# Kernel tuning notes

Hardware: AMD Instinct MI355X
Metric: run time of the kernel (lower is better)

## Reference

```python
import jax, jax.numpy as jnp
import numpy as np

N = 10000   # nodes
E = 40000   # edges
B = 250     # graphs (40 nodes each)
NODE_IN = 74
EDGE_IN = 12
H = 64      # hidden_feats
RD = 1024   # readout_feats


def setup_inputs() -> dict:
    key = jax.random.key(0)
    ks = jax.random.split(key, 32)
    w = lambda i, shape: jax.random.normal(ks[i], shape, jnp.float32) * 0.05
    inp = {
        'node_attr': jax.random.normal(ks[0], (N, NODE_IN), jnp.float32),
        'edge_attr': jax.random.normal(ks[1], (E, EDGE_IN), jnp.float32),
        'src': jax.random.randint(ks[2], (E,), 0, N, jnp.int32),
        'dst': jax.random.randint(ks[3], (E,), 0, N, jnp.int32),
        'graph_ids': (jnp.arange(N, dtype=jnp.int32) // (N // B)),
        'num_graphs': B,
        # project_node_feats: Linear(NODE_IN, H)
        'Wp': w(4, (H, NODE_IN)), 'bp': w(5, (H,)),
        # FALayer gate: Linear(2H, 1)
        'Wg': w(6, (1, 2 * H)), 'bg': w(7, (1,)),
        # edge_network: Linear(EDGE_IN + 1, H*H)
        'We': w(8, (H * H, EDGE_IN + 1)), 'be': w(9, (H * H,)),
        'nnconv_bias': w(10, (H,)),
        # GRU(H, H), single layer
        'gru_wih': w(11, (3 * H, H)), 'gru_whh': w(12, (3 * H, H)),
        'gru_bih': w(13, (3 * H,)), 'gru_bhh': w(14, (3 * H,)),
        # Set2Set LSTM: input 4H -> hidden 2H
        'lstm_wih': w(15, (8 * H, 4 * H)), 'lstm_whh': w(16, (8 * H, 2 * H)),
        'lstm_bih': w(17, (8 * H,)), 'lstm_bhh': w(18, (8 * H,)),
        # sparsify: Linear(4H, RD) + PReLU
        'Ws': w(19, (RD, 4 * H)), 'bs': w(20, (RD,)),
        'prelu_a': jnp.asarray(0.25, jnp.float32),
    }
    return inp


def _seg_softmax(e, ids, num):
    m = jax.ops.segment_max(e, ids, num_segments=num)
    ex = jnp.exp(e - m[ids])
    den = jax.ops.segment_sum(ex, ids, num_segments=num)
    return ex / den[ids]


def _forward(node_attr, edge_attr, src, dst, graph_ids, num_graphs,
             Wp, bp, Wg, bg, We, be, nnconv_bias,
             gru_wih, gru_whh, gru_bih, gru_bhh,
             lstm_wih, lstm_whh, lstm_bih, lstm_bhh,
             Ws, bs, prelu_a):
    n = node_attr.shape[0]
    h0 = jax.nn.relu(node_attr @ Wp.T + bp)            # (N, H)

    # FALayer (eval mode: dropout is identity)
    deg = jax.ops.segment_sum(jnp.ones(src.shape[0], node_attr.dtype), dst,
                              num_segments=n)           # in-degrees (N,)
    h2 = jnp.concatenate([h0[dst], h0[src]], axis=1)    # (E, 2H)
    t = jnp.tanh(h2 @ Wg.T + bg)[:, 0]                  # (E,)
    e_gate = 0.3 + t * deg[dst] * deg[src]              # (E,)
    efeat = jnp.concatenate([edge_attr, e_gate[:, None]], axis=-1)  # (E, EDGE_IN+1)

    # NNConv per-edge dynamic weights (edge_feats fixed across steps)
    W_edge = (efeat @ We.T + be).reshape(-1, H, H)      # (E, H, H)

    h = h0
    hid = h0  # GRU hidden state
    for _ in range(3):  # num_step_message_passing
        m = jnp.einsum('ei,eio->eo', h[src], W_edge)    # per-edge matvec
        agg = jax.ops.segment_sum(m, dst, num_segments=n) + nnconv_bias
        x = jax.nn.relu(agg)
        # torch GRU (gate order r, z, n)
        gi = x @ gru_wih.T + gru_bih
        gh = hid @ gru_whh.T + gru_bhh
        r = jax.nn.sigmoid(gi[:, :H] + gh[:, :H])
        z = jax.nn.sigmoid(gi[:, H:2 * H] + gh[:, H:2 * H])
        ng = jnp.tanh(gi[:, 2 * H:] + r * gh[:, 2 * H:])
        hid = (1.0 - z) * ng + z * hid
        h = hid

    feat = jnp.concatenate([h0, h], axis=1)             # (N, 2H)
    D = 2 * H

    # Set2Set readout (LSTM gate order i, f, g, o)
    q_star = jnp.zeros((num_graphs, 2 * D), feat.dtype)
    hl = jnp.zeros((num_graphs, D), feat.dtype)
    cl = jnp.zeros((num_graphs, D), feat.dtype)
    for _ in range(3):  # num_step_set2set
        g4 = q_star @ lstm_wih.T + lstm_bih + hl @ lstm_whh.T + lstm_bhh
        i = jax.nn.sigmoid(g4[:, :D])
        f = jax.nn.sigmoid(g4[:, D:2 * D])
        gg = jnp.tanh(g4[:, 2 * D:3 * D])
        o = jax.nn.sigmoid(g4[:, 3 * D:])
        cl = f * cl + i * gg
        hl = o * jnp.tanh(cl)
        q = hl                                           # (B, D)
        sc = jnp.sum(feat * q[graph_ids], axis=-1)       # (N,)
        alpha = _seg_softmax(sc, graph_ids, num_graphs)
        readout = jax.ops.segment_sum(feat * alpha[:, None], graph_ids,
                                      num_segments=num_graphs)  # (B, D)
        q_star = jnp.concatenate([q, readout], axis=-1)  # (B, 2D)

    out = q_star @ Ws.T + bs
    return jnp.where(out >= 0, out, prelu_a * out)       # PReLU


def reference(node_attr, edge_attr, src, dst, graph_ids, num_graphs,
              Wp, bp, Wg, bg, We, be, nnconv_bias,
              gru_wih, gru_whh, gru_bih, gru_bhh,
              lstm_wih, lstm_whh, lstm_bih, lstm_bhh,
              Ws, bs, prelu_a):
    return _forward(node_attr, edge_attr, src, dst, graph_ids, num_graphs,
                    Wp, bp, Wg, bg, We, be, nnconv_bias,
                    gru_wih, gru_whh, gru_bih, gru_bhh,
                    lstm_wih, lstm_whh, lstm_bih, lstm_bhh,
                    Ws, bs, prelu_a)
```

## Files before the change

kernel.cpp:

```cpp
#include <hip/hip_runtime.h>
#include <math.h>


#define H 64
#define NODE_IN 74
#define EDGE_IN 12
#define EF 14
#define GCAP 256
#define MGH 1088

__device__ __forceinline__ float sigmoidf(float x) {
    return 1.0f / (1.0f + expf(-x));
}

template<int AOP>
__global__ __launch_bounds__(256)
void gemm128_k(const float* __restrict__ A, int lda,
               const float* __restrict__ B, int ldb,
               float* __restrict__ C, int ldc,
               int M, int N, int K,
               const float* __restrict__ abias)
{
    __shared__ float sA[64][132];
    __shared__ float sB[64][68];

    const int tid = threadIdx.x;
    const int bm  = blockIdx.x * 128;
    const int bn  = blockIdx.y * 64;
    const int tx  = tid & 15;
    const int ty  = tid >> 4;

    float acc[8][4] = {{0.f}};

    for (int k0 = 0; k0 < K; k0 += 64) {
        #pragma unroll
        for (int t = 0; t < 8; ++t) {
            int idx = tid + t * 256;
            int r   = idx >> 4;
            int c   = (idx & 15) << 2;
            float4 v = {0.f, 0.f, 0.f, 0.f};
            int gm = bm + r;
            if (gm < M) {
                v = *reinterpret_cast<const float4*>(A + (size_t)gm * lda + (k0 + c));
                if (AOP == 1) {
                    v.x = fmaxf(v.x + abias[k0 + c + 0], 0.f);
                    v.y = fmaxf(v.y + abias[k0 + c + 1], 0.f);
                    v.z = fmaxf(v.z + abias[k0 + c + 2], 0.f);
                    v.w = fmaxf(v.w + abias[k0 + c + 3], 0.f);
                }
            }
            sA[c + 0][r] = v.x;
            sA[c + 1][r] = v.y;
            sA[c + 2][r] = v.z;
            sA[c + 3][r] = v.w;
        }
        #pragma unroll
        for (int t = 0; t < 4; ++t) {
            int idx = tid + t * 256;
            int r   = idx >> 4;
            int c   = (idx & 15) << 2;
            *reinterpret_cast<float4*>(&sB[r][c]) =
                *reinterpret_cast<const float4*>(B + (size_t)(k0 + r) * ldb + (bn + c));
        }
        __syncthreads();

        #pragma unroll
        for (int kk = 0; kk < 64; ++kk) {
            float4 a0 = *reinterpret_cast<const float4*>(&sA[kk][ty * 8]);
            float4 a1 = *reinterpret_cast<const float4*>(&sA[kk][ty * 8 + 4]);
            float4 bv = *reinterpret_cast<const float4*>(&sB[kk][tx * 4]);
            float ar[8] = {a0.x, a0.y, a0.z, a0.w, a1.x, a1.y, a1.z, a1.w};
            float br[4] = {bv.x, bv.y, bv.z, bv.w};
            #pragma unroll
            for (int i = 0; i < 8; ++i)
                #pragma unroll
                for (int j = 0; j < 4; ++j)
                    acc[i][j] = fmaf(ar[i], br[j], acc[i][j]);
        }
        __syncthreads();
    }

    #pragma unroll
    for (int i = 0; i < 8; ++i) {
        int gm = bm + ty * 8 + i;
        if (gm < M) {
            float4 v = {acc[i][0], acc[i][1], acc[i][2], acc[i][3]};
            *reinterpret_cast<float4*>(C + (size_t)gm * ldc + bn + tx * 4) = v;
        }
    }
}

template<int EOP>
__global__ __launch_bounds__(256)
void gemm_k(const float* __restrict__ A, int lda,
            const float* __restrict__ B, int ldb,
            float* __restrict__ C, int ldc,
            int M, int N, int K,
            const float* __restrict__ cbias,
            const float* __restrict__ prelu_a)
{
    __shared__ float sA[64][68];
    __shared__ float sB[64][68];

    const int tid = threadIdx.x;
    const int bm  = blockIdx.x * 64;
    const int bn  = blockIdx.y * 64;
    const int tx  = tid & 15;
    const int ty  = tid >> 4;

    float acc[4][4] = {{0.f}};

    for (int k0 = 0; k0 < K; k0 += 64) {
        #pragma unroll
        for (int t = 0; t < 4; ++t) {
            int idx = tid + t * 256;
            int r   = idx >> 4;
            int c   = (idx & 15) << 2;
            float4 v = {0.f, 0.f, 0.f, 0.f};
            int gm = bm + r;
            if (gm < M)
                v = *reinterpret_cast<const float4*>(A + (size_t)gm * lda + (k0 + c));
            sA[c + 0][r] = v.x;
            sA[c + 1][r] = v.y;
            sA[c + 2][r] = v.z;
            sA[c + 3][r] = v.w;
        }
        #pragma unroll
        for (int t = 0; t < 4; ++t) {
            int idx = tid + t * 256;
            int r   = idx >> 4;
            int c   = (idx & 15) << 2;
            *reinterpret_cast<float4*>(&sB[r][c]) =
                *reinterpret_cast<const float4*>(B + (size_t)(k0 + r) * ldb + (bn + c));
        }
        __syncthreads();

        #pragma unroll
        for (int kk = 0; kk < 64; ++kk) {
            float4 av = *reinterpret_cast<const float4*>(&sA[kk][ty * 4]);
            float4 bv = *reinterpret_cast<const float4*>(&sB[kk][tx * 4]);
            float ar[4] = {av.x, av.y, av.z, av.w};
            float br[4] = {bv.x, bv.y, bv.z, bv.w};
            #pragma unroll
            for (int i = 0; i < 4; ++i)
                #pragma unroll
                for (int j = 0; j < 4; ++j)
                    acc[i][j] = fmaf(ar[i], br[j], acc[i][j]);
        }
        __syncthreads();
    }

    float pa = (EOP == 1) ? prelu_a[0] : 0.f;
    #pragma unroll
    for (int i = 0; i < 4; ++i) {
        int gm = bm + ty * 4 + i;
        if (gm < M) {
            float4 v;
            float* vv = reinterpret_cast<float*>(&v);
            #pragma unroll
            for (int j = 0; j < 4; ++j) {
                float c = acc[i][j];
                if (EOP == 1) {
                    c += cbias[bn + tx * 4 + j];
                    c = (c >= 0.f) ? c : pa * c;
                }
                vv[j] = c;
            }
            *reinterpret_cast<float4*>(C + (size_t)gm * ldc + bn + tx * 4) = v;
        }
    }
}

__global__ __launch_bounds__(256)
void prep_all_k(const float* __restrict__ na, const float* __restrict__ Wp,
                const float* __restrict__ bp, float* __restrict__ h0,
                const float* __restrict__ We, const float* __restrict__ be,
                const float* __restrict__ wih, const float* __restrict__ whh,
                const float* __restrict__ lwih, const float* __restrict__ lwhh,
                const float* __restrict__ Ws,
                float* __restrict__ We2b, float* __restrict__ wihT,
                float* __restrict__ WlT, float* __restrict__ WsT,
                const int* __restrict__ dst, float* __restrict__ deg,
                int* __restrict__ icnt,
                const int* __restrict__ gid, int* __restrict__ gcnt,
                int* __restrict__ glist,
                int N, int E,
                int nb_h0, int nb_prep, int nb_deg)
{
    int b   = blockIdx.x;
    int tid = threadIdx.x;
    if (b < nb_h0) {
        int idx = b * 256 + tid;
        if (idx >= N * H) return;
        int n = idx >> 6, o = idx & 63;
        const float* x = na + (size_t)n * NODE_IN;
        const float* w = Wp + (size_t)o * NODE_IN;
        float acc = bp[o];
        #pragma unroll
        for (int k = 0; k < NODE_IN; ++k) acc = fmaf(x[k], w[k], acc);
        h0[idx] = fmaxf(acc, 0.f);
    } else if (b < nb_h0 + nb_prep) {
        int t = (b - nb_h0) * 256 + tid;
        if (t < 69632) {
            int i = t / MGH, j = t % MGH;
            float v;
            if (j < 896) {
                int k = j >> 6, o = j & 63;
                v = (k < 13) ? We[(size_t)(i * 64 + o) * 13 + k] : be[i * 64 + o];
            } else {
                int jj = j - 896;
                v = whh[(size_t)jj * 64 + i];
            }
            We2b[t] = v;
        } else if (t < 81920) {
            int u = t - 69632;
            int i = u / 192, j = u % 192;
            wihT[u] = wih[(size_t)j * 64 + i];
        } else if (t < 278528) {
            int u = t - 81920;
            int k = u >> 9, j = u & 511;
            WlT[u] = (k < 256) ? lwih[(size_t)j * 256 + k]
                               : lwhh[(size_t)j * 128 + (k - 256)];
        } else if (t < 540672) {
            int u = t - 278528;
            int k = u >> 10, j = u & 1023;
            WsT[u] = Ws[(size_t)j * 256 + k];
        }
    } else if (b < nb_h0 + nb_prep + nb_deg) {
        int e = (b - nb_h0 - nb_prep) * 256 + tid;
        if (e < E) {
            int d = dst[e];
            atomicAdd(&deg[d], 1.0f);
            atomicAdd(&icnt[d], 1);
        }
    } else {
        int n = (b - nb_h0 - nb_prep - nb_deg) * 256 + tid;
        if (n < N) {
            int g = gid[n];
            int p = atomicAdd(&gcnt[g], 1);
            if (p < GCAP) glist[(size_t)g * GCAP + p] = n;
        }
    }
}

__global__ __launch_bounds__(1024)
void scan_k(const int* __restrict__ icnt, int* __restrict__ row_ptr,
            int* __restrict__ cursor, int N)
{
    __shared__ int s[1024];
    __shared__ int carry;
    int tid = threadIdx.x;
    if (tid == 0) { carry = 0; row_ptr[0] = 0; }
    __syncthreads();
    for (int base = 0; base < N; base += 1024) {
        int i = base + tid;
        int v = (i < N) ? icnt[i] : 0;
        s[tid] = v;
        __syncthreads();
        for (int off = 1; off < 1024; off <<= 1) {
            int t = (tid >= off) ? s[tid - off] : 0;
            __syncthreads();
            s[tid] += t;
            __syncthreads();
        }
        int incl = s[tid] + carry;
        if (i < N) { row_ptr[i + 1] = incl; cursor[i] = incl - v; }
        __syncthreads();
        if (tid == 1023) carry = incl;
        __syncthreads();
    }
}

__global__ __launch_bounds__(256)
void gate_k(const float* __restrict__ h0, const float* __restrict__ ea,
            const int* __restrict__ src, const int* __restrict__ dst,
            const float* __restrict__ Wg, const float* __restrict__ bg,
            const float* __restrict__ deg, float* __restrict__ ef,
            int* __restrict__ cursor, int* __restrict__ csr_eid, int E)
{
    int e    = blockIdx.x * 4 + (threadIdx.x >> 6);
    int lane = threadIdx.x & 63;
    if (e >= E) return;
    int s = src[e], d = dst[e];
    float v = Wg[lane]      * h0[(size_t)d * H + lane]
            + Wg[H + lane]  * h0[(size_t)s * H + lane];
    #pragma unroll
    for (int off = 32; off; off >>= 1) v += __shfl_xor(v, off);
    if (lane < EF) {
        float out;
        if (lane < EDGE_IN) out = ea[(size_t)e * EDGE_IN + lane];
        else if (lane == EDGE_IN) {
            float t = tanhf(v + bg[0]);
            out = 0.3f + t * deg[d] * deg[s];
        } else out = 1.0f;
        ef[(size_t)e * EF + lane] = out;
    } else if (lane == EF) {
        int pos = atomicAdd(&cursor[d], 1);
        csr_eid[pos] = e;
    }
}

__global__ __launch_bounds__(256)
void agg_csr_k(const float* __restrict__ M, const float* __restrict__ ef,
               const int* __restrict__ src, const int* __restrict__ csr_eid,
               const int* __restrict__ row_ptr, float* __restrict__ agg, int N)
{
    int n    = blockIdx.x * 4 + (threadIdx.x >> 6);
    int lane = threadIdx.x & 63;
    if (n >= N) return;
    int p0 = row_ptr[n], p1 = row_ptr[n + 1];
    float a = 0.f;
    for (int p = p0; p < p1; ++p) {
        int e = csr_eid[p];
        int s = src[e];
        const float* Ms = M + (size_t)s * MGH + lane;
        const float* f  = ef + (size_t)e * EF;
        #pragma unroll
        for (int k = 0; k < EF; ++k) a = fmaf(f[k], Ms[k * H], a);
    }
    agg[(size_t)n * H + lane] = a;
}

__global__ __launch_bounds__(256)
void gru_k(const float* __restrict__ gi, const float* __restrict__ gh, int ghld,
           const float* __restrict__ bih, const float* __restrict__ bhh,
           const float* __restrict__ hin, float* __restrict__ hout, int N)
{
    int idx = blockIdx.x * 256 + threadIdx.x;
    if (idx >= N * H) return;
    int n = idx >> 6, o = idx & 63;
    const float* gin = gi + (size_t)n * 192;
    const float* ghn = gh + (size_t)n * ghld;
    float r  = sigmoidf(gin[o]       + bih[o]       + ghn[o]       + bhh[o]);
    float z  = sigmoidf(gin[64 + o]  + bih[64 + o]  + ghn[64 + o]  + bhh[64 + o]);
    float gn = ghn[128 + o] + bhh[128 + o];
    float ng = tanhf(gin[128 + o] + bih[128 + o] + r * gn);
    float hv = hin[idx];
    hout[idx] = (1.f - z) * ng + z * hv;
}

__global__ __launch_bounds__(64)
void att_k(const float* __restrict__ h0, const float* __restrict__ h,
           const float* __restrict__ g4,
           const float* __restrict__ lbih, const float* __restrict__ lbhh,
           float* __restrict__ cl,
           const int* __restrict__ glist, const int* __restrict__ gcnt,
           float* __restrict__ Acat)
{
    int b    = blockIdx.x;
    int lane = threadIdx.x;
    __shared__ float q[128];
    __shared__ float sc[GCAP];

    const float* g = g4 + (size_t)b * 512;
    #pragma unroll
    for (int t = 0; t < 2; ++t) {
        int d = lane + t * 64;
        float ii = sigmoidf(g[d]       + lbih[d]       + lbhh[d]);
        float ff = sigmoidf(g[128 + d] + lbih[128 + d] + lbhh[128 + d]);
        float gg = tanhf  (g[256 + d] + lbih[256 + d] + lbhh[256 + d]);
        float oo = sigmoidf(g[384 + d] + lbih[384 + d] + lbhh[384 + d]);
        float c  = ff * cl[(size_t)b * 128 + d] + ii * gg;
        cl[(size_t)b * 128 + d] = c;
        q[d] = oo * tanhf(c);
    }
    __syncthreads();

    int c = gcnt[b]; if (c > GCAP) c = GCAP;

    float lmax = -INFINITY;
    for (int i = lane; i < c; i += 64) {
        int n = glist[(size_t)b * GCAP + i];
        const float* f0 = h0 + (size_t)n * H;
        const float* f1 = h  + (size_t)n * H;
        float s = 0.f;
        #pragma unroll
        for (int j = 0; j < H; ++j) s = fmaf(f0[j], q[j], s);
        #pragma unroll
        for (int j = 0; j < H; ++j) s = fmaf(f1[j], q[H + j], s);
        sc[i] = s;
        lmax = fmaxf(lmax, s);
    }
    #pragma unroll
    for (int off = 32; off; off >>= 1) lmax = fmaxf(lmax, __shfl_xor(lmax, off));

    float lsum = 0.f;
    for (int i = lane; i < c; i += 64) {
        float e = expf(sc[i] - lmax);
        sc[i] = e;
        lsum += e;
    }
    #pragma unroll
    for (int off = 32; off; off >>= 1) lsum += __shfl_xor(lsum, off);
    __syncthreads();

    float inv = 1.f / lsum;
    float r0 = 0.f, r1 = 0.f;
    for (int i = 0; i < c; ++i) {
        int n = glist[(size_t)b * GCAP + i];
        float w = sc[i];
        r0 = fmaf(w, h0[(size_t)n * H + lane], r0);
        r1 = fmaf(w, h [(size_t)n * H + lane], r1);
    }
    float* A = Acat + (size_t)b * 384;
    A[lane]       = q[lane];
    A[64 + lane]  = q[64 + lane];
    A[128 + lane] = r0 * inv;
    A[192 + lane] = r1 * inv;
    A[256 + lane] = q[lane];
    A[320 + lane] = q[64 + lane];
}

extern "C" void kernel_launch(void* const* d_in, const int* in_sizes, int n_in,
                              void* d_out, int out_size, void* d_ws, size_t ws_size,
                              hipStream_t stream)
{
    (void)n_in; (void)ws_size;
    const float* node_attr = (const float*)d_in[0];
    const float* edge_attr = (const float*)d_in[1];
    const int*   src       = (const int*)d_in[2];
    const int*   dst       = (const int*)d_in[3];
    const int*   gid       = (const int*)d_in[4];
    const float* Wp        = (const float*)d_in[6];
    const float* bp        = (const float*)d_in[7];
    const float* Wg        = (const float*)d_in[8];
    const float* bg        = (const float*)d_in[9];
    const float* We        = (const float*)d_in[10];
    const float* be        = (const float*)d_in[11];
    const float* nb        = (const float*)d_in[12];
    const float* gwih      = (const float*)d_in[13];
    const float* gwhh      = (const float*)d_in[14];
    const float* gbih      = (const float*)d_in[15];
    const float* gbhh      = (const float*)d_in[16];
    const float* lwih      = (const float*)d_in[17];
    const float* lwhh      = (const float*)d_in[18];
    const float* lbih      = (const float*)d_in[19];
    const float* lbhh      = (const float*)d_in[20];
    const float* Ws        = (const float*)d_in[21];
    const float* bs        = (const float*)d_in[22];
    const float* pa        = (const float*)d_in[23];

    const int N = in_sizes[0] / NODE_IN;
    const int E = in_sizes[2];
    const int B = out_size / 1024;

    float* ws = (float*)d_ws;
    size_t off = 0;
    auto alloc = [&](size_t n) { size_t o = off; off += (n + 63) & ~(size_t)63; return o; };
    size_t oDEG  = alloc(N);
    size_t oICNT = alloc(N);
    size_t oCL   = alloc((size_t)B * 128);
    size_t oACAT = alloc((size_t)B * 384);
    size_t oGCNT = alloc(B);
    size_t zero_beg = oDEG, zero_end = off;
    size_t oRP   = alloc(N + 1);
    size_t oCUR  = alloc(N);
    size_t oCSR  = alloc(E);
    size_t oAGG  = alloc((size_t)N * H);
    size_t oH0   = alloc((size_t)N * H);
    size_t oHB   = alloc((size_t)N * H);
    size_t oEF   = alloc((size_t)E * EF);
    size_t oGL   = alloc((size_t)B * GCAP);
    size_t oWE2  = alloc(64 * MGH);
    size_t oWIHT = alloc(64 * 192);
    size_t oWLT  = alloc(384 * 512);
    size_t oWST  = alloc(256 * 1024);
    size_t oG4   = alloc((size_t)B * 512);
    size_t oGI   = alloc((size_t)N * 192);
    size_t oM    = alloc((size_t)N * MGH);

    float* deg   = ws + oDEG;
    int*   icnt  = (int*)(ws + oICNT);
    float* clb   = ws + oCL;
    float* Acat  = ws + oACAT;
    int*   gcnt  = (int*)(ws + oGCNT);
    int*   rowp  = (int*)(ws + oRP);
    int*   cursor= (int*)(ws + oCUR);
    int*   csr   = (int*)(ws + oCSR);
    float* agg   = ws + oAGG;
    float* h0    = ws + oH0;
    float* hbuf  = ws + oHB;
    float* ef    = ws + oEF;
    int*   glist = (int*)(ws + oGL);
    float* We2b  = ws + oWE2;
    float* wihT  = ws + oWIHT;
    float* WlT   = ws + oWLT;
    float* WsT   = ws + oWST;
    float* g4    = ws + oG4;
    float* gib   = ws + oGI;
    float* Mb    = ws + oM;
    float* ghb   = Mb + 896;

    const int mt128 = (N + 127) / 128;
    const int bt    = (B + 63) / 64;

    hipMemsetAsync(ws + zero_beg, 0, (zero_end - zero_beg) * sizeof(float), stream);
    const int nb_h0   = (N * H + 255) / 256;
    const int nb_prep = (540672 + 255) / 256;
    const int nb_deg  = (E + 255) / 256;
    const int nb_gl   = (N + 255) / 256;
    prep_all_k<<<nb_h0 + nb_prep + nb_deg + nb_gl, 256, 0, stream>>>(
        node_attr, Wp, bp, h0, We, be, gwih, gwhh, lwih, lwhh, Ws,
        We2b, wihT, WlT, WsT, dst, deg, icnt, gid, gcnt, glist,
        N, E, nb_h0, nb_prep, nb_deg);
    scan_k<<<1, 1024, 0, stream>>>(icnt, rowp, cursor, N);
    gate_k<<<(E + 3) / 4, 256, 0, stream>>>(h0, edge_attr, src, dst, Wg, bg, deg,
                                            ef, cursor, csr, E);

    const float* hcur = h0;
    for (int step = 0; step < 3; ++step) {
        gemm128_k<0><<<dim3(mt128, MGH / 64), 256, 0, stream>>>(
            hcur, H, We2b, MGH, Mb, MGH, N, MGH, 64, nullptr);
        agg_csr_k<<<(N + 3) / 4, 256, 0, stream>>>(Mb, ef, src, csr, rowp, agg, N);
        gemm128_k<1><<<dim3(mt128, 3), 256, 0, stream>>>(
            agg, H, wihT, 192, gib, 192, N, 192, 64, nb);
        gru_k<<<(N * H + 255) / 256, 256, 0, stream>>>(gib, ghb, MGH, gbih, gbhh,
                                                       hcur, hbuf, N);
        hcur = hbuf;
    }

    for (int s = 0; s < 3; ++s) {
        gemm_k<0><<<dim3(bt, 8), 256, 0, stream>>>(Acat, 384, WlT, 512, g4, 512,
                                                   B, 512, 384, nullptr, nullptr);
        att_k<<<B, 64, 0, stream>>>(h0, hbuf, g4, lbih, lbhh, clb, glist, gcnt, Acat);
    }

    gemm_k<1><<<dim3(bt, 16), 256, 0, stream>>>(Acat, 384, WsT, 1024, (float*)d_out, 1024,
                                                B, 1024, 256, bs, pa);
}
```

Baseline: 474.4 us.

## Reassociate NNConv as sparse edge-feature gather then dense weight GEMM

The NNConv message computation is reordered. Each node now aggregates edge-feature-weighted neighbour hidden states into a 14x64 tensor G, and G is multiplied by the edge-network weights in a split-K GEMM, replacing the per-node 1088-wide projection followed by a per-edge gather. The GRU input and hidden GEMMs are issued as one launch, the LSTM gate GEMM is fused into a 256-thread attention kernel, and the CSR scan is rewritten with wavefront shuffles. This avoids writing and re-reading the large N x 1088 intermediate, at the cost of an N x 896 G buffer and more scattered per-edge work.

```diff
diff --git a/kernel.cpp b/kernel.cpp
--- a/kernel.cpp
+++ b/kernel.cpp
@@ -7,107 +7,26 @@
 #define EDGE_IN 12
 #define EF 14
 #define GCAP 256
-#define MGH 1088
 
 __device__ __forceinline__ float sigmoidf(float x) {
     return 1.0f / (1.0f + expf(-x));
 }
 
-template<int AOP>
-__global__ __launch_bounds__(256)
-void gemm128_k(const float* __restrict__ A, int lda,
-               const float* __restrict__ B, int ldb,
-               float* __restrict__ C, int ldc,
-               int M, int N, int K,
-               const float* __restrict__ abias)
-{
-    __shared__ float sA[64][132];
-    __shared__ float sB[64][68];
-
-    const int tid = threadIdx.x;
-    const int bm  = blockIdx.x * 128;
-    const int bn  = blockIdx.y * 64;
-    const int tx  = tid & 15;
-    const int ty  = tid >> 4;
-
-    float acc[8][4] = {{0.f}};
-
-    for (int k0 = 0; k0 < K; k0 += 64) {
-        #pragma unroll
-        for (int t = 0; t < 8; ++t) {
-            int idx = tid + t * 256;
-            int r   = idx >> 4;
-            int c   = (idx & 15) << 2;
-            float4 v = {0.f, 0.f, 0.f, 0.f};
-            int gm = bm + r;
-            if (gm < M) {
-                v = *reinterpret_cast<const float4*>(A + (size_t)gm * lda + (k0 + c));
-                if (AOP == 1) {
-                    v.x = fmaxf(v.x + abias[k0 + c + 0], 0.f);
-                    v.y = fmaxf(v.y + abias[k0 + c + 1], 0.f);
-                    v.z = fmaxf(v.z + abias[k0 + c + 2], 0.f);
-                    v.w = fmaxf(v.w + abias[k0 + c + 3], 0.f);
-                }
-            }
-            sA[c + 0][r] = v.x;
-            sA[c + 1][r] = v.y;
-            sA[c + 2][r] = v.z;
-            sA[c + 3][r] = v.w;
-        }
-        #pragma unroll
-        for (int t = 0; t < 4; ++t) {
-            int idx = tid + t * 256;
-            int r   = idx >> 4;
-            int c   = (idx & 15) << 2;
-            *reinterpret_cast<float4*>(&sB[r][c]) =
-                *reinterpret_cast<const float4*>(B + (size_t)(k0 + r) * ldb + (bn + c));
-        }
-        __syncthreads();
-
-        #pragma unroll
-        for (int kk = 0; kk < 64; ++kk) {
-            float4 a0 = *reinterpret_cast<const float4*>(&sA[kk][ty * 8]);
-            float4 a1 = *reinterpret_cast<const float4*>(&sA[kk][ty * 8 + 4]);
-            float4 bv = *reinterpret_cast<const float4*>(&sB[kk][tx * 4]);
-            float ar[8] = {a0.x, a0.y, a0.z, a0.w, a1.x, a1.y, a1.z, a1.w};
-            float br[4] = {bv.x, bv.y, bv.z, bv.w};
-            #pragma unroll
-            for (int i = 0; i < 8; ++i)
-                #pragma unroll
-                for (int j = 0; j < 4; ++j)
-                    acc[i][j] = fmaf(ar[i], br[j], acc[i][j]);
-        }
-        __syncthreads();
-    }
-
-    #pragma unroll
-    for (int i = 0; i < 8; ++i) {
-        int gm = bm + ty * 8 + i;
-        if (gm < M) {
-            float4 v = {acc[i][0], acc[i][1], acc[i][2], acc[i][3]};
-            *reinterpret_cast<float4*>(C + (size_t)gm * ldc + bn + tx * 4) = v;
-        }
-    }
-}
-
-template<int EOP>
-__global__ __launch_bounds__(256)
-void gemm_k(const float* __restrict__ A, int lda,
-            const float* __restrict__ B, int ldb,
-            float* __restrict__ C, int ldc,
-            int M, int N, int K,
-            const float* __restrict__ cbias,
-            const float* __restrict__ prelu_a)
+__global__ __launch_bounds__(256)
+void gemm_prelu_k(const float* __restrict__ A, int lda,
+                  const float* __restrict__ B, int ldb,
+                  float* __restrict__ C, int ldc,
+                  int M, int N, int K,
+                  const float* __restrict__ cbias,
+                  const float* __restrict__ prelu_a)
 {
     __shared__ float sA[64][68];
     __shared__ float sB[64][68];
-
     const int tid = threadIdx.x;
     const int bm  = blockIdx.x * 64;
     const int bn  = blockIdx.y * 64;
     const int tx  = tid & 15;
     const int ty  = tid >> 4;
-
     float acc[4][4] = {{0.f}};
 
     for (int k0 = 0; k0 < K; k0 += 64) {
@@ -120,10 +39,8 @@
             int gm = bm + r;
             if (gm < M)
                 v = *reinterpret_cast<const float4*>(A + (size_t)gm * lda + (k0 + c));
-            sA[c + 0][r] = v.x;
-            sA[c + 1][r] = v.y;
-            sA[c + 2][r] = v.z;
-            sA[c + 3][r] = v.w;
+            sA[c + 0][r] = v.x; sA[c + 1][r] = v.y;
+            sA[c + 2][r] = v.z; sA[c + 3][r] = v.w;
         }
         #pragma unroll
         for (int t = 0; t < 4; ++t) {
@@ -134,7 +51,6 @@
                 *reinterpret_cast<const float4*>(B + (size_t)(k0 + r) * ldb + (bn + c));
         }
         __syncthreads();
-
         #pragma unroll
         for (int kk = 0; kk < 64; ++kk) {
             float4 av = *reinterpret_cast<const float4*>(&sA[kk][ty * 4]);
@@ -150,7 +66,7 @@
         __syncthreads();
     }
 
-    float pa = (EOP == 1) ? prelu_a[0] : 0.f;
+    float pa = prelu_a[0];
     #pragma unroll
     for (int i = 0; i < 4; ++i) {
         int gm = bm + ty * 4 + i;
@@ -159,15 +75,140 @@
             float* vv = reinterpret_cast<float*>(&v);
             #pragma unroll
             for (int j = 0; j < 4; ++j) {
-                float c = acc[i][j];
-                if (EOP == 1) {
-                    c += cbias[bn + tx * 4 + j];
-                    c = (c >= 0.f) ? c : pa * c;
-                }
-                vv[j] = c;
+                float c = acc[i][j] + cbias[bn + tx * 4 + j];
+                vv[j] = (c >= 0.f) ? c : pa * c;
             }
             *reinterpret_cast<float4*>(C + (size_t)gm * ldc + bn + tx * 4) = v;
         }
+    }
+}
+
+__global__ __launch_bounds__(256)
+void aggg_k(const float* __restrict__ G, const float* __restrict__ W2n,
+            float* __restrict__ agg0, float* __restrict__ agg1, int M)
+{
+    __shared__ float sA[64][68];
+    __shared__ float sB[64][68];
+    const int tid = threadIdx.x;
+    const int bm  = blockIdx.x * 64;
+    const int z   = blockIdx.z;
+    const int tx  = tid & 15;
+    const int ty  = tid >> 4;
+    float* C = z ? agg1 : agg0;
+    float acc[4][4] = {{0.f}};
+
+    for (int k0 = z * 448; k0 < z * 448 + 448; k0 += 64) {
+        #pragma unroll
+        for (int t = 0; t < 4; ++t) {
+            int idx = tid + t * 256;
+            int r   = idx >> 4;
+            int c   = (idx & 15) << 2;
+            float4 v = {0.f, 0.f, 0.f, 0.f};
+            int gm = bm + r;
+            if (gm < M)
+                v = *reinterpret_cast<const float4*>(G + (size_t)gm * 896 + (k0 + c));
+            sA[c + 0][r] = v.x; sA[c + 1][r] = v.y;
+            sA[c + 2][r] = v.z; sA[c + 3][r] = v.w;
+        }
+        #pragma unroll
+        for (int t = 0; t < 4; ++t) {
+            int idx = tid + t * 256;
+            int r   = idx >> 4;
+            int c   = (idx & 15) << 2;
+            *reinterpret_cast<float4*>(&sB[r][c]) =
+                *reinterpret_cast<const float4*>(W2n + (size_t)(k0 + r) * 64 + c);
+        }
+        __syncthreads();
+        #pragma unroll
+        for (int kk = 0; kk < 64; ++kk) {
+            float4 av = *reinterpret_cast<const float4*>(&sA[kk][ty * 4]);
+            float4 bv = *reinterpret_cast<const float4*>(&sB[kk][tx * 4]);
+            float ar[4] = {av.x, av.y, av.z, av.w};
+            float br[4] = {bv.x, bv.y, bv.z, bv.w};
+            #pragma unroll
+            for (int i = 0; i < 4; ++i)
+                #pragma unroll
+                for (int j = 0; j < 4; ++j)
+                    acc[i][j] = fmaf(ar[i], br[j], acc[i][j]);
+        }
+        __syncthreads();
+    }
+    #pragma unroll
+    for (int i = 0; i < 4; ++i) {
+        int gm = bm + ty * 4 + i;
+        if (gm < M)
+            *reinterpret_cast<float4*>(C + (size_t)gm * 64 + tx * 4) =
+                make_float4(acc[i][0], acc[i][1], acc[i][2], acc[i][3]);
+    }
+}
+
+__global__ __launch_bounds__(256)
+void gigh_k(const float* __restrict__ agg0, const float* __restrict__ agg1,
+            const float* __restrict__ nb, const float* __restrict__ h,
+            const float* __restrict__ wihT, const float* __restrict__ whhT,
+            float* __restrict__ gib, float* __restrict__ ghb, int M)
+{
+    __shared__ float sA[64][68];
+    __shared__ float sB[64][68];
+    const int tid = threadIdx.x;
+    const int bm  = blockIdx.x * 64;
+    const int bn  = blockIdx.y * 64;
+    const int z   = blockIdx.z;
+    const int tx  = tid & 15;
+    const int ty  = tid >> 4;
+    const float* Bm = z ? whhT : wihT;
+    float* C = z ? ghb : gib;
+    float acc[4][4] = {{0.f}};
+
+    #pragma unroll
+    for (int t = 0; t < 4; ++t) {
+        int idx = tid + t * 256;
+        int r   = idx >> 4;
+        int c   = (idx & 15) << 2;
+        float4 v = {0.f, 0.f, 0.f, 0.f};
+        int gm = bm + r;
+        if (gm < M) {
+            if (z == 0) {
+                float4 a0 = *reinterpret_cast<const float4*>(agg0 + (size_t)gm * 64 + c);
+                float4 a1 = *reinterpret_cast<const float4*>(agg1 + (size_t)gm * 64 + c);
+                v.x = fmaxf(a0.x + a1.x + nb[c + 0], 0.f);
+                v.y = fmaxf(a0.y + a1.y + nb[c + 1], 0.f);
+                v.z = fmaxf(a0.z + a1.z + nb[c + 2], 0.f);
+                v.w = fmaxf(a0.w + a1.w + nb[c + 3], 0.f);
+            } else {
+                v = *reinterpret_cast<const float4*>(h + (size_t)gm * 64 + c);
+            }
+        }
+        sA[c + 0][r] = v.x; sA[c + 1][r] = v.y;
+        sA[c + 2][r] = v.z; sA[c + 3][r] = v.w;
+    }
+    #pragma unroll
+    for (int t = 0; t < 4; ++t) {
+        int idx = tid + t * 256;
+        int r   = idx >> 4;
+        int c   = (idx & 15) << 2;
+        *reinterpret_cast<float4*>(&sB[r][c]) =
+            *reinterpret_cast<const float4*>(Bm + (size_t)r * 192 + (bn + c));
+    }
+    __syncthreads();
+    #pragma unroll
+    for (int kk = 0; kk < 64; ++kk) {
+        float4 av = *reinterpret_cast<const float4*>(&sA[kk][ty * 4]);
+        float4 bv = *reinterpret_cast<const float4*>(&sB[kk][tx * 4]);
+        float ar[4] = {av.x, av.y, av.z, av.w};
+        float br[4] = {bv.x, bv.y, bv.z, bv.w};
+        #pragma unroll
+        for (int i = 0; i < 4; ++i)
+            #pragma unroll
+            for (int j = 0; j < 4; ++j)
+                acc[i][j] = fmaf(ar[i], br[j], acc[i][j]);
+    }
+    #pragma unroll
+    for (int i = 0; i < 4; ++i) {
+        int gm = bm + ty * 4 + i;
+        if (gm < M)
+            *reinterpret_cast<float4*>(C + (size_t)gm * 192 + bn + tx * 4) =
+                make_float4(acc[i][0], acc[i][1], acc[i][2], acc[i][3]);
     }
 }
 
@@ -178,8 +219,9 @@
                 const float* __restrict__ wih, const float* __restrict__ whh,
                 const float* __restrict__ lwih, const float* __restrict__ lwhh,
                 const float* __restrict__ Ws,
-                float* __restrict__ We2b, float* __restrict__ wihT,
-                float* __restrict__ WlT, float* __restrict__ WsT,
+                float* __restrict__ W2n, float* __restrict__ wihT,
+                float* __restrict__ whhT, float* __restrict__ WlT,
+                float* __restrict__ WsT,
                 const int* __restrict__ dst, float* __restrict__ deg,
                 int* __restrict__ icnt,
                 const int* __restrict__ gid, int* __restrict__ gcnt,
@@ -201,21 +243,18 @@
         h0[idx] = fmaxf(acc, 0.f);
     } else if (b < nb_h0 + nb_prep) {
         int t = (b - nb_h0) * 256 + tid;
-        if (t < 69632) {
-            int i = t / MGH, j = t % MGH;
-            float v;
-            if (j < 896) {
-                int k = j >> 6, o = j & 63;
-                v = (k < 13) ? We[(size_t)(i * 64 + o) * 13 + k] : be[i * 64 + o];
-            } else {
-                int jj = j - 896;
-                v = whh[(size_t)jj * 64 + i];
-            }
-            We2b[t] = v;
+        if (t < 57344) {
+            int ko = t >> 6, o = t & 63;
+            int k = ko >> 6, i = ko & 63;
+            W2n[t] = (k < 13) ? We[(size_t)(i * 64 + o) * 13 + k] : be[i * 64 + o];
+        } else if (t < 69632) {
+            int u = t - 57344;
+            int i = u / 192, j = u % 192;
+            wihT[u] = wih[(size_t)j * 64 + i];
         } else if (t < 81920) {
             int u = t - 69632;
             int i = u / 192, j = u % 192;
-            wihT[u] = wih[(size_t)j * 64 + i];
+            whhT[u] = whh[(size_t)j * 64 + i];
         } else if (t < 278528) {
             int u = t - 81920;
             int k = u >> 9, j = u & 511;
@@ -247,26 +286,39 @@
 void scan_k(const int* __restrict__ icnt, int* __restrict__ row_ptr,
             int* __restrict__ cursor, int N)
 {
-    __shared__ int s[1024];
-    __shared__ int carry;
-    int tid = threadIdx.x;
-    if (tid == 0) { carry = 0; row_ptr[0] = 0; }
+    __shared__ int wsum[16];
+    __shared__ int carrySh;
+    int tid  = threadIdx.x;
+    int lane = tid & 63;
+    int wid  = tid >> 6;
+    if (tid == 0) { carrySh = 0; row_ptr[0] = 0; }
     __syncthreads();
     for (int base = 0; base < N; base += 1024) {
         int i = base + tid;
         int v = (i < N) ? icnt[i] : 0;
-        s[tid] = v;
-        __syncthreads();
-        for (int off = 1; off < 1024; off <<= 1) {
-            int t = (tid >= off) ? s[tid - off] : 0;
-            __syncthreads();
-            s[tid] += t;
-            __syncthreads();
-        }
-        int incl = s[tid] + carry;
+        int x = v;
+        #pragma unroll
+        for (int off = 1; off < 64; off <<= 1) {
+            int t = __shfl_up(x, off);
+            if (lane >= off) x += t;
+        }
+        if (lane == 63) wsum[wid] = x;
+        __syncthreads();
+        if (wid == 0) {
+            int s = (lane < 16) ? wsum[lane] : 0;
+            #pragma unroll
+            for (int off = 1; off < 16; off <<= 1) {
+                int t = __shfl_up(s, off);
+                if (lane >= off) s += t;
+            }
+            if (lane < 16) wsum[lane] = s;
+        }
+        __syncthreads();
+        int woff = (wid > 0) ? wsum[wid - 1] : 0;
+        int incl = x + woff + carrySh;
         if (i < N) { row_ptr[i + 1] = incl; cursor[i] = incl - v; }
         __syncthreads();
-        if (tid == 1023) carry = incl;
+        if (tid == 1023) carrySh = incl;
         __syncthreads();
     }
 }
@@ -301,28 +353,31 @@
 }
 
 __global__ __launch_bounds__(256)
-void agg_csr_k(const float* __restrict__ M, const float* __restrict__ ef,
+void sparseG_k(const float* __restrict__ h, const float* __restrict__ ef,
                const int* __restrict__ src, const int* __restrict__ csr_eid,
-               const int* __restrict__ row_ptr, float* __restrict__ agg, int N)
+               const int* __restrict__ rowp, float* __restrict__ G, int N)
 {
     int n    = blockIdx.x * 4 + (threadIdx.x >> 6);
     int lane = threadIdx.x & 63;
     if (n >= N) return;
-    int p0 = row_ptr[n], p1 = row_ptr[n + 1];
-    float a = 0.f;
+    float g[EF];
+    #pragma unroll
+    for (int k = 0; k < EF; ++k) g[k] = 0.f;
+    int p0 = rowp[n], p1 = rowp[n + 1];
     for (int p = p0; p < p1; ++p) {
         int e = csr_eid[p];
-        int s = src[e];
-        const float* Ms = M + (size_t)s * MGH + lane;
-        const float* f  = ef + (size_t)e * EF;
-        #pragma unroll
-        for (int k = 0; k < EF; ++k) a = fmaf(f[k], Ms[k * H], a);
-    }
-    agg[(size_t)n * H + lane] = a;
-}
-
-__global__ __launch_bounds__(256)
-void gru_k(const float* __restrict__ gi, const float* __restrict__ gh, int ghld,
+        float hv = h[(size_t)src[e] * H + lane];
+        const float* f = ef + (size_t)e * EF;
+        #pragma unroll
+        for (int k = 0; k < EF; ++k) g[k] = fmaf(f[k], hv, g[k]);
+    }
+    float* Gr = G + (size_t)n * (EF * H);
+    #pragma unroll
+    for (int k = 0; k < EF; ++k) Gr[k * H + lane] = g[k];
+}
+
+__global__ __launch_bounds__(256)
+void gru_k(const float* __restrict__ gi, const float* __restrict__ gh,
            const float* __restrict__ bih, const float* __restrict__ bhh,
            const float* __restrict__ hin, float* __restrict__ hout, int N)
 {
@@ -330,7 +385,7 @@
     if (idx >= N * H) return;
     int n = idx >> 6, o = idx & 63;
     const float* gin = gi + (size_t)n * 192;
-    const float* ghn = gh + (size_t)n * ghld;
+    const float* ghn = gh + (size_t)n * 192;
     float r  = sigmoidf(gin[o]       + bih[o]       + ghn[o]       + bhh[o]);
     float z  = sigmoidf(gin[64 + o]  + bih[64 + o]  + ghn[64 + o]  + bhh[64 + o]);
     float gn = ghn[128 + o] + bhh[128 + o];
@@ -339,27 +394,41 @@
     hout[idx] = (1.f - z) * ng + z * hv;
 }
 
-__global__ __launch_bounds__(64)
-void att_k(const float* __restrict__ h0, const float* __restrict__ h,
-           const float* __restrict__ g4,
-           const float* __restrict__ lbih, const float* __restrict__ lbhh,
-           float* __restrict__ cl,
-           const int* __restrict__ glist, const int* __restrict__ gcnt,
-           float* __restrict__ Acat)
+__global__ __launch_bounds__(256)
+void att256_k(const float* __restrict__ h0, const float* __restrict__ h,
+              const float* __restrict__ WlT,
+              const float* __restrict__ lbih, const float* __restrict__ lbhh,
+              float* __restrict__ cl,
+              const int* __restrict__ glist, const int* __restrict__ gcnt,
+              float* __restrict__ Acat)
 {
     int b    = blockIdx.x;
-    int lane = threadIdx.x;
+    int tid  = threadIdx.x;
+    int lane = tid & 63;
+    int wid  = tid >> 6;
+    __shared__ float acatS[384];
+    __shared__ float g4s[512];
     __shared__ float q[128];
     __shared__ float sc[GCAP];
-
-    const float* g = g4 + (size_t)b * 512;
-    #pragma unroll
-    for (int t = 0; t < 2; ++t) {
-        int d = lane + t * 64;
-        float ii = sigmoidf(g[d]       + lbih[d]       + lbhh[d]);
-        float ff = sigmoidf(g[128 + d] + lbih[128 + d] + lbhh[128 + d]);
-        float gg = tanhf  (g[256 + d] + lbih[256 + d] + lbhh[256 + d]);
-        float oo = sigmoidf(g[384 + d] + lbih[384 + d] + lbhh[384 + d]);
+    __shared__ float red[8];
+
+    for (int j = tid; j < 384; j += 256) acatS[j] = Acat[(size_t)b * 384 + j];
+    __syncthreads();
+
+    for (int j = tid; j < 512; j += 256) {
+        float s = 0.f;
+        for (int k = 0; k < 384; ++k)
+            s = fmaf(acatS[k], WlT[(size_t)k * 512 + j], s);
+        g4s[j] = s;
+    }
+    __syncthreads();
+
+    if (tid < 128) {
+        int d = tid;
+        float ii = sigmoidf(g4s[d]       + lbih[d]       + lbhh[d]);
+        float ff = sigmoidf(g4s[128 + d] + lbih[128 + d] + lbhh[128 + d]);
+        float gg = tanhf  (g4s[256 + d] + lbih[256 + d] + lbhh[256 + d]);
+        float oo = sigmoidf(g4s[384 + d] + lbih[384 + d] + lbhh[384 + d]);
         float c  = ff * cl[(size_t)b * 128 + d] + ii * gg;
         cl[(size_t)b * 128 + d] = c;
         q[d] = oo * tanhf(c);
@@ -369,46 +438,45 @@
     int c = gcnt[b]; if (c > GCAP) c = GCAP;
 
     float lmax = -INFINITY;
-    for (int i = lane; i < c; i += 64) {
+    for (int i = wid; i < c; i += 4) {
         int n = glist[(size_t)b * GCAP + i];
-        const float* f0 = h0 + (size_t)n * H;
-        const float* f1 = h  + (size_t)n * H;
-        float s = 0.f;
-        #pragma unroll
-        for (int j = 0; j < H; ++j) s = fmaf(f0[j], q[j], s);
-        #pragma unroll
-        for (int j = 0; j < H; ++j) s = fmaf(f1[j], q[H + j], s);
-        sc[i] = s;
-        lmax = fmaxf(lmax, s);
-    }
-    #pragma unroll
-    for (int off = 32; off; off >>= 1) lmax = fmaxf(lmax, __shfl_xor(lmax, off));
+        float v = h0[(size_t)n * H + lane] * q[lane]
+                + h [(size_t)n * H + lane] * q[64 + lane];
+        #pragma unroll
+        for (int off = 32; off; off >>= 1) v += __shfl_xor(v, off);
+        if (lane == 0) sc[i] = v;
+        lmax = fmaxf(lmax, v);
+    }
+    if (lane == 0) red[wid] = lmax;
+    __syncthreads();
+    lmax = fmaxf(fmaxf(red[0], red[1]), fmaxf(red[2], red[3]));
 
     float lsum = 0.f;
-    for (int i = lane; i < c; i += 64) {
+    for (int i = tid; i < c; i += 256) {
         float e = expf(sc[i] - lmax);
         sc[i] = e;
         lsum += e;
     }
     #pragma unroll
     for (int off = 32; off; off >>= 1) lsum += __shfl_xor(lsum, off);
+    if (lane == 0) red[4 + wid] = lsum;
     __syncthreads();
-
-    float inv = 1.f / lsum;
-    float r0 = 0.f, r1 = 0.f;
-    for (int i = 0; i < c; ++i) {
-        int n = glist[(size_t)b * GCAP + i];
-        float w = sc[i];
-        r0 = fmaf(w, h0[(size_t)n * H + lane], r0);
-        r1 = fmaf(w, h [(size_t)n * H + lane], r1);
+    float inv = 1.f / (red[4] + red[5] + red[6] + red[7]);
+
+    float r = 0.f;
+    if (tid < 128) {
+        const float* srcf = (tid < 64) ? h0 : h;
+        for (int i = 0; i < c; ++i) {
+            int n = glist[(size_t)b * GCAP + i];
+            r = fmaf(sc[i], srcf[(size_t)n * H + lane], r);
+        }
     }
     float* A = Acat + (size_t)b * 384;
-    A[lane]       = q[lane];
-    A[64 + lane]  = q[64 + lane];
-    A[128 + lane] = r0 * inv;
-    A[192 + lane] = r1 * inv;
-    A[256 + lane] = q[lane];
-    A[320 + lane] = q[64 + lane];
+    if (tid < 128) {
+        A[tid]       = q[tid];
+        A[128 + tid] = r * inv;
+        A[256 + tid] = q[tid];
+    }
 }
 
 extern "C" void kernel_launch(void* const* d_in, const int* in_sizes, int n_in,
@@ -456,18 +524,20 @@
     size_t oRP   = alloc(N + 1);
     size_t oCUR  = alloc(N);
     size_t oCSR  = alloc(E);
-    size_t oAGG  = alloc((size_t)N * H);
     size_t oH0   = alloc((size_t)N * H);
     size_t oHB   = alloc((size_t)N * H);
     size_t oEF   = alloc((size_t)E * EF);
     size_t oGL   = alloc((size_t)B * GCAP);
-    size_t oWE2  = alloc(64 * MGH);
+    size_t oW2N  = alloc(896 * 64);
     size_t oWIHT = alloc(64 * 192);
+    size_t oWHHT = alloc(64 * 192);
     size_t oWLT  = alloc(384 * 512);
     size_t oWST  = alloc(256 * 1024);
-    size_t oG4   = alloc((size_t)B * 512);
+    size_t oAGG0 = alloc((size_t)N * 64);
+    size_t oAGG1 = alloc((size_t)N * 64);
     size_t oGI   = alloc((size_t)N * 192);
-    size_t oM    = alloc((size_t)N * MGH);
+    size_t oGH   = alloc((size_t)N * 192);
+    size_t oG    = alloc((size_t)N * (EF * H));
 
     float* deg   = ws + oDEG;
     int*   icnt  = (int*)(ws + oICNT);
@@ -477,22 +547,23 @@
     int*   rowp  = (int*)(ws + oRP);
     int*   cursor= (int*)(ws + oCUR);
     int*   csr   = (int*)(ws + oCSR);
-    float* agg   = ws + oAGG;
     float* h0    = ws + oH0;
     float* hbuf  = ws + oHB;
     float* ef    = ws + oEF;
     int*   glist = (int*)(ws + oGL);
-    float* We2b  = ws + oWE2;
+    float* W2n   = ws + oW2N;
     float* wihT  = ws + oWIHT;
+    float* whhT  = ws + oWHHT;
     float* WlT   = ws + oWLT;
     float* WsT   = ws + oWST;
-    float* g4    = ws + oG4;
+    float* agg0  = ws + oAGG0;
+    float* agg1  = ws + oAGG1;
     float* gib   = ws + oGI;
-    float* Mb    = ws + oM;
-    float* ghb   = Mb + 896;
-
-    const int mt128 = (N + 127) / 128;
-    const int bt    = (B + 63) / 64;
+    float* ghb   = ws + oGH;
+    float* Gb    = ws + oG;
+
+    const int mt64 = (N + 63) / 64;
+    const int bt   = (B + 63) / 64;
 
     hipMemsetAsync(ws + zero_beg, 0, (zero_end - zero_beg) * sizeof(float), stream);
     const int nb_h0   = (N * H + 255) / 256;
@@ -501,7 +572,7 @@
     const int nb_gl   = (N + 255) / 256;
     prep_all_k<<<nb_h0 + nb_prep + nb_deg + nb_gl, 256, 0, stream>>>(
         node_attr, Wp, bp, h0, We, be, gwih, gwhh, lwih, lwhh, Ws,
-        We2b, wihT, WlT, WsT, dst, deg, icnt, gid, gcnt, glist,
+        W2n, wihT, whhT, WlT, WsT, dst, deg, icnt, gid, gcnt, glist,
         N, E, nb_h0, nb_prep, nb_deg);
     scan_k<<<1, 1024, 0, stream>>>(icnt, rowp, cursor, N);
     gate_k<<<(E + 3) / 4, 256, 0, stream>>>(h0, edge_attr, src, dst, Wg, bg, deg,
@@ -509,22 +580,21 @@
 
     const float* hcur = h0;
     for (int step = 0; step < 3; ++step) {
-        gemm128_k<0><<<dim3(mt128, MGH / 64), 256, 0, stream>>>(
-            hcur, H, We2b, MGH, Mb, MGH, N, MGH, 64, nullptr);
-        agg_csr_k<<<(N + 3) / 4, 256, 0, stream>>>(Mb, ef, src, csr, rowp, agg, N);
-        gemm128_k<1><<<dim3(mt128, 3), 256, 0, stream>>>(
-            agg, H, wihT, 192, gib, 192, N, 192, 64, nb);
-        gru_k<<<(N * H + 255) / 256, 256, 0, stream>>>(gib, ghb, MGH, gbih, gbhh,
+        sparseG_k<<<(N + 3) / 4, 256, 0, stream>>>(hcur, ef, src, csr, rowp, Gb, N);
+        aggg_k<<<dim3(mt64, 1, 2), 256, 0, stream>>>(Gb, W2n, agg0, agg1, N);
+        gigh_k<<<dim3(mt64, 3, 2), 256, 0, stream>>>(agg0, agg1, nb, hcur,
+                                                     wihT, whhT, gib, ghb, N);
+        gru_k<<<(N * H + 255) / 256, 256, 0, stream>>>(gib, ghb, gbih, gbhh,
                                                        hcur, hbuf, N);
         hcur = hbuf;
     }
 
     for (int s = 0; s < 3; ++s) {
-        gemm_k<0><<<dim3(bt, 8), 256, 0, stream>>>(Acat, 384, WlT, 512, g4, 512,
-                                                   B, 512, 384, nullptr, nullptr);
-        att_k<<<B, 64, 0, stream>>>(h0, hbuf, g4, lbih, lbhh, clb, glist, gcnt, Acat);
-    }
-
-    gemm_k<1><<<dim3(bt, 16), 256, 0, stream>>>(Acat, 384, WsT, 1024, (float*)d_out, 1024,
-                                                B, 1024, 256, bs, pa);
-}
+        att256_k<<<B, 256, 0, stream>>>(h0, hbuf, WlT, lbih, lbhh, clb,
+                                        glist, gcnt, Acat);
+    }
+
+    gemm_prelu_k<<<dim3(bt, 16), 256, 0, stream>>>(Acat, 384, WsT, 1024,
+                                                   (float*)d_out, 1024,
+                                                   B, 1024, 256, bs, pa);
+}
```

Result: slower. 501.9 us (+5.8%).
